# Performance work log

Hardware: AMD Instinct MI355X
Metric: run time of the kernel (lower is better)

## Reference

```python
import jax, jax.numpy as jnp
import numpy as np

B, T, E, H, V = 64, 128, 256, 1024, 8000

def setup_inputs() -> dict:
    key = jax.random.key(0)
    ks = jax.random.split(key, 18)
    s = 0.1
    f = lambda k, shp: (jax.random.normal(k, shp) * s).astype(jnp.float32)
    return {
        "x": jax.random.randint(ks[0], (B, T), 0, V),
        "given_num": 64,
        "emb": f(ks[1], (V, E)),
        "Wi": f(ks[2], (E, H)), "Ui": f(ks[3], (H, H)), "bi": f(ks[4], (H,)),
        "Wf": f(ks[5], (E, H)), "Uf": f(ks[6], (H, H)), "bf": f(ks[7], (H,)),
        "Wog": f(ks[8], (E, H)), "Uog": f(ks[9], (H, H)), "bog": f(ks[10], (H,)),
        "Wc": f(ks[11], (E, H)), "Uc": f(ks[12], (H, H)), "bc": f(ks[13], (H,)),
        "Wo": f(ks[14], (H, V)), "bo": f(ks[15], (V,)),
    }

def reference(x, given_num, emb, Wi, Ui, bi, Wf, Uf, bf, Wog, Uog, bog, Wc, Uc, bc, Wo, bo):
    # NOTE: the torch source overwrites processed_x[i] AFTER it has been consumed,
    # so the recurrence is fully teacher-forced on x; sampling only fills gen_x
    # for steps >= given_num. We reproduce exactly that.
    px = jnp.transpose(emb[x], (1, 0, 2))               # [T,B,E] teacher embeddings
    Wcat = jnp.concatenate([Wi, Wf, Wog, Wc], axis=1)    # [E,4H] fused input-gate weights
    Ucat = jnp.concatenate([Ui, Uf, Uog, Uc], axis=1)    # [H,4H] fused hidden-gate weights
    bcat = jnp.concatenate([bi, bf, bog, bc])            # [4H]
    xw = jnp.einsum('tbe,eh->tbh', px, Wcat) + bcat      # [T,B,4H] one big GEMM upfront
    keys = jax.random.split(jax.random.key(1), T)        # per-step sampling keys

    def step(carry, inp):
        h, c = carry
        xw_t, i, xtok, k = inp
        z = xw_t + h @ Ucat                              # [B,4H] fused gate pre-activations
        i_g, f_g, o_g, c_hat = jnp.split(z, 4, axis=-1)
        c = jax.nn.sigmoid(f_g) * c + jax.nn.sigmoid(i_g) * jnp.tanh(c_hat)
        h = jax.nn.sigmoid(o_g) * jnp.tanh(c)
        logits = h @ Wo + bo                             # [B,V]
        samp = jax.random.categorical(k, logits)         # = multinomial over softmax
        tok = jnp.where(i < given_num, xtok, samp)
        return (h, c), tok

    h0 = jnp.zeros((B, H), jnp.float32)
    c0 = jnp.zeros((B, H), jnp.float32)
    _, toks = jax.lax.scan(step, (h0, c0), (xw, jnp.arange(T), x.T, keys))
    return toks.T                                        # [B,T] int tokens (gen_x)
```

## Files before the change

### kernel.cpp

```cpp
#include <hip/hip_runtime.h>
#include <hip/hip_cooperative_groups.h>
#include <cstdint>
#include <cstddef>

#define TT 128
#define BB 64
#define EE 256
#define HH 1024
#define VV 8000
#define LSTRIDE 132

__device__ __forceinline__ uint32_t rotl32(uint32_t v, int r){ return (v<<r)|(v>>(32-r)); }

__device__ __forceinline__ void tf2x32(uint32_t k0, uint32_t k1, uint32_t x0, uint32_t x1,
                                       uint32_t& y0, uint32_t& y1)
{
  const uint32_t k2 = k0 ^ k1 ^ 0x1BD11BDAu;
  x0 += k0; x1 += k1;
#define TFR(r) { x0 += x1; x1 = rotl32(x1,(r)); x1 ^= x0; }
  TFR(13) TFR(15) TFR(26) TFR(6)   x0 += k1; x1 += k2 + 1u;
  TFR(17) TFR(29) TFR(16) TFR(24)  x0 += k2; x1 += k0 + 2u;
  TFR(13) TFR(15) TFR(26) TFR(6)   x0 += k0; x1 += k1 + 3u;
  TFR(17) TFR(29) TFR(16) TFR(24)  x0 += k1; x1 += k2 + 4u;
  TFR(13) TFR(15) TFR(26) TFR(6)   x0 += k2; x1 += k0 + 5u;
#undef TFR
  y0 = x0; y1 = x1;
}

__device__ __forceinline__ float u01f(uint32_t bits){
  float f = __uint_as_float((bits >> 9) | 0x3f800000u) - 1.0f;
  return (f == 0.0f) ? 1.17549435e-38f : f;
}

__device__ __forceinline__ float xla_tanh(float x){
  float xc = fminf(fmaxf(x, -7.90531110763549805f), 7.90531110763549805f);
  float x2 = __fmul_rn(xc, xc);
  float num = -2.76076847742355e-16f;
  num = __fadd_rn(__fmul_rn(x2, num),  2.00018790482477e-13f);
  num = __fadd_rn(__fmul_rn(x2, num), -8.60467152213735e-11f);
  num = __fadd_rn(__fmul_rn(x2, num),  5.12229709037114e-08f);
  num = __fadd_rn(__fmul_rn(x2, num),  1.48572235717979e-05f);
  num = __fadd_rn(__fmul_rn(x2, num),  6.37261928875436e-04f);
  num = __fadd_rn(__fmul_rn(x2, num),  4.89352455891786e-03f);
  num = __fmul_rn(xc, num);
  float den = 1.19825839466702e-06f;
  den = __fadd_rn(__fmul_rn(x2, den), 1.18534705686654e-04f);
  den = __fadd_rn(__fmul_rn(x2, den), 2.26843463243900e-03f);
  den = __fadd_rn(__fmul_rn(x2, den), 4.89352518554385e-03f);
  float r = __fdiv_rn(num, den);
  return (fabsf(x) < 0.0004f) ? x : r;
}

__device__ __forceinline__ float xla_sigmoid(float x){
  float t = xla_tanh(__fmul_rn(0.5f, x));
  return __fadd_rn(0.5f, __fmul_rn(0.5f, t));
}

__device__ __forceinline__ unsigned long long pack32(float s, int v){
  uint32_t u = __float_as_uint(s);
  u = (u >> 31) ? ~u : (u | 0x80000000u);
  return ((unsigned long long)u << 32) | (unsigned)(8191 - v);
}

#define LGKM0 asm volatile("s_waitcnt lgkmcnt(0)" ::: "memory")

__global__ void initz(float* hfull, unsigned long long* best, int* flags){
  int i = blockIdx.x*256 + threadIdx.x;
  if (i < HH*BB)  hfull[i] = 0.f;
  if (i < TT*BB)  best[i] = 0ull;
  if (i < 256)    flags[i] = 0;
}

__global__ __launch_bounds__(256) void pxgen(
    const int* __restrict__ x, const float* __restrict__ emb, float* __restrict__ px)
{
  int flat = blockIdx.x*256 + threadIdx.x;
  int b = flat & 63;
  int e = (flat >> 6) & 255;
  int t = flat >> 14;
  if (t >= TT) return;
  int tok = x[b*TT + t];
  px[((size_t)t*EE + e)*BB + b] = emb[(size_t)tok*EE + e];
}

__global__ __launch_bounds__(256) void transpose4f(
    const float* __restrict__ g0, const float* __restrict__ g1,
    const float* __restrict__ g2, const float* __restrict__ g3,
    float* __restrict__ out, int R, int C)
{
  const float* in = (blockIdx.y==0)?g0:(blockIdx.y==1)?g1:(blockIdx.y==2)?g2:g3;
  int tilesC = C >> 6;
  int tr = blockIdx.x / tilesC, tc = blockIdx.x % tilesC;
  __shared__ float tile[64][65];
  int tid = threadIdx.x;
  #pragma unroll
  for (int s = 0; s < 16; ++s) {
    int li = s*256 + tid;
    int r = li >> 6, c = li & 63;
    tile[r][c] = in[(size_t)(tr*64 + r)*C + tc*64 + c];
  }
  __syncthreads();
  #pragma unroll
  for (int s = 0; s < 16; ++s) {
    int li = s*256 + tid;
    int c = li >> 6, r = li & 63;
    out[((size_t)blockIdx.y*C + tc*64 + c)*R + tr*64 + r] = tile[r][c];
  }
}

__global__ __launch_bounds__(512, 2) void lstm_rec(
    const float* __restrict__ Wt, const float* __restrict__ Ut,
    const float* __restrict__ bi, const float* __restrict__ bf,
    const float* __restrict__ bog, const float* __restrict__ bc,
    const float* __restrict__ px, float* __restrict__ hfull,
    int* __restrict__ flags)
{
  __shared__ float sA[64*LSTRIDE];
  __shared__ float sB[64*LSTRIDE];
  __shared__ float spx[64*LSTRIDE];
  __shared__ float xch[512];

  const int tid  = threadIdx.x;
  const int w    = tid >> 6;
  const int lane = tid & 63;
  const int p    = w >> 1;
  const int half = w & 1;
  const int ju   = __builtin_amdgcn_readfirstlane(blockIdx.x*4 + p);
  const int g0   = 2*half, g1 = 2*half + 1;
  const int sw4  = ((lane >> 3) & 7) << 2;

  const float* U0 = Ut + ((size_t)g0*HH + ju)*HH;
  const float* U1 = Ut + ((size_t)g1*HH + ju)*HH;
  const float* W0 = Wt + ((size_t)g0*HH + ju)*EE;
  const float* W1 = Wt + ((size_t)g1*HH + ju)*EE;
  const float biaA = half ? bog[ju] : bi[ju];
  const float biaB = half ? bc[ju]  : bf[ju];

  float c = 0.f;
  float B0 = 0.f, B1 = 0.f;
  float4 pre[4];

  auto load_chunk = [&](const float* hp, int hcn){
    #pragma unroll
    for (int s = 0; s < 4; ++s) {
      int f = s*512 + tid;
      int k = f >> 4, b0 = (f & 15)*4;
      pre[s] = *(const float4*)(hp + (size_t)(hcn*128 + k)*BB + b0);
    }
  };
  auto store_chunk = [&](float* buf){
    #pragma unroll
    for (int s = 0; s < 4; ++s) {
      int f = s*512 + tid;
      int k = f >> 4, b0 = (f & 15)*4;
      int kc = k ^ (((b0 >> 3) & 7) << 2);
      buf[(b0+0)*LSTRIDE + kc] = pre[s].x;
      buf[(b0+1)*LSTRIDE + kc] = pre[s].y;
      buf[(b0+2)*LSTRIDE + kc] = pre[s].z;
      buf[(b0+3)*LSTRIDE + kc] = pre[s].w;
    }
  };

  auto compute_xw = [&](int t2){
    float A0 = 0.f, A1 = 0.f;
    #pragma unroll 1
    for (int ch = 0; ch < 2; ++ch) {
      const float* pxc = px + ((size_t)t2*EE + ch*128)*BB;
      LGKM0;
      __builtin_amdgcn_s_barrier();
      #pragma unroll
      for (int s = 0; s < 4; ++s) {
        int f = s*512 + tid;
        int e = f >> 4, b0 = (f & 15)*4;
        float4 v = *(const float4*)(pxc + (size_t)e*BB + b0);
        int ec = e ^ (((b0 >> 3) & 7) << 2);
        spx[(b0+0)*LSTRIDE + ec] = v.x;
        spx[(b0+1)*LSTRIDE + ec] = v.y;
        spx[(b0+2)*LSTRIDE + ec] = v.z;
        spx[(b0+3)*LSTRIDE + ec] = v.w;
      }
      LGKM0;
      __builtin_amdgcn_s_barrier();
      #pragma unroll
      for (int e = 0; e < 128; e += 4) {
        float4 p4 = *(const float4*)&spx[lane*LSTRIDE + (e ^ sw4)];
        A0 = __fadd_rn(A0, __fmul_rn(p4.x, W0[ch*128 + e + 0]));
        A1 = __fadd_rn(A1, __fmul_rn(p4.x, W1[ch*128 + e + 0]));
        A0 = __fadd_rn(A0, __fmul_rn(p4.y, W0[ch*128 + e + 1]));
        A1 = __fadd_rn(A1, __fmul_rn(p4.y, W1[ch*128 + e + 1]));
        A0 = __fadd_rn(A0, __fmul_rn(p4.z, W0[ch*128 + e + 2]));
        A1 = __fadd_rn(A1, __fmul_rn(p4.z, W1[ch*128 + e + 2]));
        A0 = __fadd_rn(A0, __fmul_rn(p4.w, W0[ch*128 + e + 3]));
        A1 = __fadd_rn(A1, __fmul_rn(p4.w, W1[ch*128 + e + 3]));
      }
    }
    B0 = __fadd_rn(A0, biaA);
    B1 = __fadd_rn(A1, biaB);
  };

  compute_xw(0);

  #pragma unroll 1
  for (int t = 0; t < TT; ++t) {
    const float* hp = hfull + (size_t)t*(HH*BB);
    float*       rn = hfull + (size_t)(t+1)*(HH*BB);

    load_chunk(hp, 0);
    float R0 = 0.f, R1 = 0.f, T0 = 0.f, T1 = 0.f;
    #pragma unroll 1
    for (int hc = 0; hc < 8; ++hc) {
      float* cur = (hc & 1) ? sB : sA;
      store_chunk(cur);
      if (hc < 7) load_chunk(hp, hc + 1);
      LGKM0;
      __builtin_amdgcn_s_barrier();
      #pragma unroll
      for (int sub = 0; sub < 4; ++sub) {
        int kabs = hc*128 + sub*32;
        if (kabs == 288 || kabs == 576 || kabs == 864) {
          T0 = __fadd_rn(T0, R0); R0 = 0.f;
          T1 = __fadd_rn(T1, R1); R1 = 0.f;
        }
        #pragma unroll
        for (int q = sub*32; q < sub*32 + 32; q += 4) {
          float4 h4 = *(const float4*)&cur[lane*LSTRIDE + (q ^ sw4)];
          R0 = __fadd_rn(R0, __fmul_rn(h4.x, U0[hc*128 + q + 0]));
          R1 = __fadd_rn(R1, __fmul_rn(h4.x, U1[hc*128 + q + 0]));
          R0 = __fadd_rn(R0, __fmul_rn(h4.y, U0[hc*128 + q + 1]));
          R1 = __fadd_rn(R1, __fmul_rn(h4.y, U1[hc*128 + q + 1]));
          R0 = __fadd_rn(R0, __fmul_rn(h4.z, U0[hc*128 + q + 2]));
          R1 = __fadd_rn(R1, __fmul_rn(h4.z, U1[hc*128 + q + 2]));
          R0 = __fadd_rn(R0, __fmul_rn(h4.w, U0[hc*128 + q + 3]));
          R1 = __fadd_rn(R1, __fmul_rn(h4.w, U1[hc*128 + q + 3]));
        }
      }
    }
    T0 = __fadd_rn(T0, R0);
    T1 = __fadd_rn(T1, R1);
    float z0 = __fadd_rn(B0, T0);
    float z1 = __fadd_rn(B1, T1);

    float igv = 0.f, fgv = 0.f, hv = 0.f;
    if (half) {
      float th  = xla_tanh(z1);
      float ogs = xla_sigmoid(z0);
      xch[p*64 + lane]       = th;
      xch[256 + p*64 + lane] = ogs;
    } else {
      igv = xla_sigmoid(z0);
      fgv = xla_sigmoid(z1);
    }
    LGKM0;
    __builtin_amdgcn_s_barrier();
    if (!half) {
      float th  = xch[p*64 + lane];
      float ogs = xch[256 + p*64 + lane];
      c = __fadd_rn(__fmul_rn(fgv, c), __fmul_rn(igv, th));
      hv = __fmul_rn(ogs, xla_tanh(c));
      __hip_atomic_store(&rn[(size_t)ju*BB + lane], hv,
                         __ATOMIC_RELAXED, __HIP_MEMORY_SCOPE_AGENT);
    }
    __syncthreads();
    if (tid == 0)
      __hip_atomic_store(&flags[blockIdx.x], t+1, __ATOMIC_RELEASE, __HIP_MEMORY_SCOPE_AGENT);

    if (t < TT-1) {
      compute_xw(t+1);
      if (w == 0) {
        for (;;) {
          int m0 = __hip_atomic_load(&flags[lane],       __ATOMIC_RELAXED, __HIP_MEMORY_SCOPE_AGENT);
          int m1 = __hip_atomic_load(&flags[64 + lane],  __ATOMIC_RELAXED, __HIP_MEMORY_SCOPE_AGENT);
          int m2 = __hip_atomic_load(&flags[128 + lane], __ATOMIC_RELAXED, __HIP_MEMORY_SCOPE_AGENT);
          int m3 = __hip_atomic_load(&flags[192 + lane], __ATOMIC_RELAXED, __HIP_MEMORY_SCOPE_AGENT);
          int mm = m0 < m1 ? m0 : m1;
          int nn = m2 < m3 ? m2 : m3;
          mm = mm < nn ? mm : nn;
          if (__all(mm >= t+1)) break;
          __builtin_amdgcn_s_sleep(1);
        }
        __atomic_signal_fence(__ATOMIC_ACQUIRE);
      }
      __syncthreads();
    }
  }
}

__global__ __launch_bounds__(256, 2) void logits_samp(
    const float* __restrict__ hfull, const float* __restrict__ Wo,
    const float* __restrict__ bo, const int* __restrict__ gnp,
    unsigned long long* __restrict__ best)
{
  const int t = 64 + blockIdx.y;
  if (t < gnp[0]) return;
  const int vt   = blockIdx.x;
  const int z    = blockIdx.z;
  const int tid  = threadIdx.x;
  const int w    = tid >> 6;
  const int lane = tid & 63;

  int v[4], vc[4]; bool val[4];
  #pragma unroll
  for (int vj = 0; vj < 4; ++vj) {
    v[vj]  = vt*1024 + vj*256 + tid;
    val[vj] = (v[vj] < VV);
    vc[vj] = val[vj] ? v[vj] : (VV-1);
  }

  __shared__ float hds[128*16];
  __shared__ unsigned long long red[4][16];

  float tot[64], reg[64];
  #pragma unroll
  for (int i = 0; i < 64; ++i) { tot[i] = 0.f; reg[i] = 0.f; }

  const float* hf = hfull + (size_t)(t+1)*(HH*BB);

  #pragma unroll 1
  for (int kc8 = 0; kc8 < 8; ++kc8) {
    __syncthreads();
    #pragma unroll
    for (int s = 0; s < 8; ++s) {
      int idx = s*256 + tid;
      int kl = idx >> 4, bb = idx & 15;
      hds[idx] = hf[(size_t)(kc8*128 + kl)*BB + z*16 + bb];
    }
    __syncthreads();
    #pragma unroll 1
    for (int sub = 0; sub < 4; ++sub) {
      int kabs = kc8*128 + sub*32;
      if (kabs == 288 || kabs == 576 || kabs == 864) {
        #pragma unroll
        for (int i = 0; i < 64; ++i) { tot[i] = __fadd_rn(tot[i], reg[i]); reg[i] = 0.f; }
      }
      #pragma unroll 2
      for (int k = sub*32; k < sub*32 + 32; ++k) {
        const float* wr = Wo + (size_t)(kc8*128 + k)*VV;
        float wv0 = wr[vc[0]], wv1 = wr[vc[1]], wv2 = wr[vc[2]], wv3 = wr[vc[3]];
        #pragma unroll
        for (int bb = 0; bb < 16; ++bb) {
          float hb = hds[k*16 + bb];
          reg[0*16+bb] = __fadd_rn(reg[0*16+bb], __fmul_rn(hb, wv0));
          reg[1*16+bb] = __fadd_rn(reg[1*16+bb], __fmul_rn(hb, wv1));
          reg[2*16+bb] = __fadd_rn(reg[2*16+bb], __fmul_rn(hb, wv2));
          reg[3*16+bb] = __fadd_rn(reg[3*16+bb], __fmul_rn(hb, wv3));
        }
      }
    }
  }
  #pragma unroll
  for (int i = 0; i < 64; ++i) tot[i] = __fadd_rn(tot[i], reg[i]);

  uint32_t kt0, kt1;
  tf2x32(0u, 1u, 0u, (uint32_t)t, kt0, kt1);
  float bov[4];
  #pragma unroll
  for (int vj = 0; vj < 4; ++vj) bov[vj] = val[vj] ? bo[v[vj]] : 0.f;

  #pragma unroll 1
  for (int bb = 0; bb < 16; ++bb) {
    int bglob = z*16 + bb;
    unsigned long long pm = 0ull;
    #pragma unroll
    for (int vj = 0; vj < 4; ++vj) {
      if (val[vj]) {
        uint32_t y0, y1;
        tf2x32(kt0, kt1, 0u, (uint32_t)(bglob*VV + v[vj]), y0, y1);
        float u  = u01f(y0 ^ y1);
        float l1 = logf(u);
        float l2 = logf(-l1);
        float g  = -l2;
        float L  = __fadd_rn(tot[vj*16 + bb], bov[vj]);
        float sc = __fadd_rn(g, L);
        unsigned long long pk = pack32(sc, v[vj]);
        if (pk > pm) pm = pk;
      }
    }
    #pragma unroll
    for (int m = 32; m > 0; m >>= 1) {
      unsigned long long q = __shfl_xor(pm, m);
      if (q > pm) pm = q;
    }
    if (lane == 0) red[w][bb] = pm;
    __syncthreads();
    if (tid == 0) {
      unsigned long long m0 = red[0][bb];
      if (red[1][bb] > m0) m0 = red[1][bb];
      if (red[2][bb] > m0) m0 = red[2][bb];
      if (red[3][bb] > m0) m0 = red[3][bb];
      atomicMax(&best[(size_t)t*BB + z*16 + bb], m0);
    }
    __syncthreads();
  }
}

__global__ void finalize(const int* __restrict__ x, const int* __restrict__ gnp,
                         const unsigned long long* __restrict__ best, int* __restrict__ out)
{
  int i = blockIdx.x*256 + threadIdx.x;
  if (i >= BB*TT) return;
  int t = i & 127;
  int b = i >> 7;
  if (t < gnp[0] || t < 64) out[i] = x[i];
  else out[i] = 8191 - (int)(best[(size_t)t*BB + b] & 0x1FFFull);
}

extern "C" void kernel_launch(void* const* d_in, const int* in_sizes, int n_in,
                              void* d_out, int out_size, void* d_ws, size_t ws_size,
                              hipStream_t stream)
{
  const int*   x    = (const int*)  d_in[0];
  const int*   gn   = (const int*)  d_in[1];
  const float* emb  = (const float*)d_in[2];
  const float* Wi   = (const float*)d_in[3];
  const float* Ui   = (const float*)d_in[4];
  const float* bi   = (const float*)d_in[5];
  const float* Wf   = (const float*)d_in[6];
  const float* Uf   = (const float*)d_in[7];
  const float* bf   = (const float*)d_in[8];
  const float* Wog  = (const float*)d_in[9];
  const float* Uog  = (const float*)d_in[10];
  const float* bog  = (const float*)d_in[11];
  const float* Wc   = (const float*)d_in[12];
  const float* Uc   = (const float*)d_in[13];
  const float* bc   = (const float*)d_in[14];
  const float* Wo   = (const float*)d_in[15];
  const float* bo   = (const float*)d_in[16];

  float* Ut    = (float*)d_ws;
  float* Wt    = Ut + (size_t)4*1024*1024;
  float* hfull = Wt + (size_t)1024*1024;
  float* px    = hfull + (size_t)(TT+1)*HH*BB;
  unsigned long long* best =
      (unsigned long long*)(px + (size_t)TT*EE*BB);
  int* flags  = (int*)(best + (size_t)TT*BB);

  initz<<<512, 256, 0, stream>>>(hfull, best, flags);
  transpose4f<<<dim3(256,4), 256, 0, stream>>>(Ui, Uf, Uog, Uc, Ut, 1024, 1024);
  transpose4f<<<dim3(64,4),  256, 0, stream>>>(Wi, Wf, Wog, Wc, Wt, 256, 1024);
  pxgen<<<8192, 256, 0, stream>>>(x, emb, px);

  const float* Wtp = Wt; const float* Utp = Ut;
  const float* bip = bi; const float* bfp = bf; const float* bogp = bog; const float* bcp = bc;
  const float* pxp = px; float* hfullp = hfull; int* flagsp = flags;
  void* kargs[] = { (void*)&Wtp, (void*)&Utp,
                    (void*)&bip, (void*)&bfp, (void*)&bogp, (void*)&bcp,
                    (void*)&pxp, (void*)&hfullp, (void*)&flagsp };
  hipLaunchCooperativeKernel((void*)lstm_rec, dim3(256), dim3(512), kargs, 0, stream);

  logits_samp<<<dim3(8,64,4), 256, 0, stream>>>(hfull, Wo, bo, gn, best);
  finalize<<<32, 256, 0, stream>>>(x, gn, best, (int*)d_out);
}
```

Measured before the change: 7.400 ms.

## Store h and px in lane-friendly blocked layout, drop LDS staging in recurrence

The hidden state and embedding inputs are rewritten into a blocked [t][b/16][k/4][b%16][k%4] layout, so each lane can read its float4 directly from global memory (L2). This replaces the shared-memory transpose staging, double buffering and barriers in the recurrent matvec and the input projection. A separate hist buffer in the original [k][b] layout is written for steps >= 64 so the logits kernel keeps its access pattern. The cost is more global/L2 traffic per step, with 16 redundant reads across waves, plus extra history stores.

After: 8.952 ms. 21.0% more time.

```diff
diff --git a/kernel.cpp b/kernel.cpp
--- a/kernel.cpp
+++ b/kernel.cpp
@@ -8,7 +8,6 @@
 #define EE 256
 #define HH 1024
 #define VV 8000
-#define LSTRIDE 132
 
 __device__ __forceinline__ uint32_t rotl32(uint32_t v, int r){ return (v<<r)|(v>>(32-r)); }
 
@@ -64,23 +63,24 @@
 
 #define LGKM0 asm volatile("s_waitcnt lgkmcnt(0)" ::: "memory")
 
-__global__ void initz(float* hfull, unsigned long long* best, int* flags){
+__global__ void initz(float* hT, unsigned long long* best, int* flags){
   int i = blockIdx.x*256 + threadIdx.x;
-  if (i < HH*BB)  hfull[i] = 0.f;
+  if (i < HH*BB)  hT[i] = 0.f;
   if (i < TT*BB)  best[i] = 0ull;
   if (i < 256)    flags[i] = 0;
 }
 
 __global__ __launch_bounds__(256) void pxgen(
-    const int* __restrict__ x, const float* __restrict__ emb, float* __restrict__ px)
+    const int* __restrict__ x, const float* __restrict__ emb, float* __restrict__ pxT)
 {
   int flat = blockIdx.x*256 + threadIdx.x;
-  int b = flat & 63;
-  int e = (flat >> 6) & 255;
+  int e = flat & 255;
+  int b = (flat >> 8) & 63;
   int t = flat >> 14;
   if (t >= TT) return;
   int tok = x[b*TT + t];
-  px[((size_t)t*EE + e)*BB + b] = emb[(size_t)tok*EE + e];
+  size_t fi = ((((size_t)t*4 + (b>>4))*64 + (e>>2))*16 + (size_t)(b&15))*4 + (e&3);
+  pxT[fi] = emb[(size_t)tok*EE + e];
 }
 
 __global__ __launch_bounds__(256) void transpose4f(
@@ -112,12 +112,9 @@
     const float* __restrict__ Wt, const float* __restrict__ Ut,
     const float* __restrict__ bi, const float* __restrict__ bf,
     const float* __restrict__ bog, const float* __restrict__ bc,
-    const float* __restrict__ px, float* __restrict__ hfull,
-    int* __restrict__ flags)
-{
-  __shared__ float sA[64*LSTRIDE];
-  __shared__ float sB[64*LSTRIDE];
-  __shared__ float spx[64*LSTRIDE];
+    const float* __restrict__ pxT, float* __restrict__ hT,
+    float* __restrict__ hist, int* __restrict__ flags)
+{
   __shared__ float xch[512];
 
   const int tid  = threadIdx.x;
@@ -127,7 +124,7 @@
   const int half = w & 1;
   const int ju   = __builtin_amdgcn_readfirstlane(blockIdx.x*4 + p);
   const int g0   = 2*half, g1 = 2*half + 1;
-  const int sw4  = ((lane >> 3) & 7) << 2;
+  const int lgrp = lane >> 4, l16 = lane & 15;
 
   const float* U0 = Ut + ((size_t)g0*HH + ju)*HH;
   const float* U1 = Ut + ((size_t)g1*HH + ju)*HH;
@@ -138,60 +135,25 @@
 
   float c = 0.f;
   float B0 = 0.f, B1 = 0.f;
-  float4 pre[4];
-
-  auto load_chunk = [&](const float* hp, int hcn){
-    #pragma unroll
-    for (int s = 0; s < 4; ++s) {
-      int f = s*512 + tid;
-      int k = f >> 4, b0 = (f & 15)*4;
-      pre[s] = *(const float4*)(hp + (size_t)(hcn*128 + k)*BB + b0);
-    }
-  };
-  auto store_chunk = [&](float* buf){
-    #pragma unroll
-    for (int s = 0; s < 4; ++s) {
-      int f = s*512 + tid;
-      int k = f >> 4, b0 = (f & 15)*4;
-      int kc = k ^ (((b0 >> 3) & 7) << 2);
-      buf[(b0+0)*LSTRIDE + kc] = pre[s].x;
-      buf[(b0+1)*LSTRIDE + kc] = pre[s].y;
-      buf[(b0+2)*LSTRIDE + kc] = pre[s].z;
-      buf[(b0+3)*LSTRIDE + kc] = pre[s].w;
-    }
-  };
 
   auto compute_xw = [&](int t2){
     float A0 = 0.f, A1 = 0.f;
+    const float4* pb = (const float4*)pxT + (((size_t)t2*4 + lgrp)*64)*16 + l16;
     #pragma unroll 1
-    for (int ch = 0; ch < 2; ++ch) {
-      const float* pxc = px + ((size_t)t2*EE + ch*128)*BB;
-      LGKM0;
-      __builtin_amdgcn_s_barrier();
+    for (int ec = 0; ec < 8; ++ec) {
       #pragma unroll
-      for (int s = 0; s < 4; ++s) {
-        int f = s*512 + tid;
-        int e = f >> 4, b0 = (f & 15)*4;
-        float4 v = *(const float4*)(pxc + (size_t)e*BB + b0);
-        int ec = e ^ (((b0 >> 3) & 7) << 2);
-        spx[(b0+0)*LSTRIDE + ec] = v.x;
-        spx[(b0+1)*LSTRIDE + ec] = v.y;
-        spx[(b0+2)*LSTRIDE + ec] = v.z;
-        spx[(b0+3)*LSTRIDE + ec] = v.w;
-      }
-      LGKM0;
-      __builtin_amdgcn_s_barrier();
-      #pragma unroll
-      for (int e = 0; e < 128; e += 4) {
-        float4 p4 = *(const float4*)&spx[lane*LSTRIDE + (e ^ sw4)];
-        A0 = __fadd_rn(A0, __fmul_rn(p4.x, W0[ch*128 + e + 0]));
-        A1 = __fadd_rn(A1, __fmul_rn(p4.x, W1[ch*128 + e + 0]));
-        A0 = __fadd_rn(A0, __fmul_rn(p4.y, W0[ch*128 + e + 1]));
-        A1 = __fadd_rn(A1, __fmul_rn(p4.y, W1[ch*128 + e + 1]));
-        A0 = __fadd_rn(A0, __fmul_rn(p4.z, W0[ch*128 + e + 2]));
-        A1 = __fadd_rn(A1, __fmul_rn(p4.z, W1[ch*128 + e + 2]));
-        A0 = __fadd_rn(A0, __fmul_rn(p4.w, W0[ch*128 + e + 3]));
-        A1 = __fadd_rn(A1, __fmul_rn(p4.w, W1[ch*128 + e + 3]));
+      for (int j = 0; j < 8; ++j) {
+        int eq = ec*8 + j;
+        float4 v = pb[(size_t)eq*16];
+        int e = eq*4;
+        A0 = __fadd_rn(A0, __fmul_rn(v.x, W0[e+0]));
+        A1 = __fadd_rn(A1, __fmul_rn(v.x, W1[e+0]));
+        A0 = __fadd_rn(A0, __fmul_rn(v.y, W0[e+1]));
+        A1 = __fadd_rn(A1, __fmul_rn(v.y, W1[e+1]));
+        A0 = __fadd_rn(A0, __fmul_rn(v.z, W0[e+2]));
+        A1 = __fadd_rn(A1, __fmul_rn(v.z, W1[e+2]));
+        A0 = __fadd_rn(A0, __fmul_rn(v.w, W0[e+3]));
+        A1 = __fadd_rn(A1, __fmul_rn(v.w, W1[e+3]));
       }
     }
     B0 = __fadd_rn(A0, biaA);
@@ -202,18 +164,10 @@
 
   #pragma unroll 1
   for (int t = 0; t < TT; ++t) {
-    const float* hp = hfull + (size_t)t*(HH*BB);
-    float*       rn = hfull + (size_t)(t+1)*(HH*BB);
-
-    load_chunk(hp, 0);
+    const float4* hb = (const float4*)hT + (((size_t)t*4 + lgrp)*256)*16 + l16;
     float R0 = 0.f, R1 = 0.f, T0 = 0.f, T1 = 0.f;
     #pragma unroll 1
     for (int hc = 0; hc < 8; ++hc) {
-      float* cur = (hc & 1) ? sB : sA;
-      store_chunk(cur);
-      if (hc < 7) load_chunk(hp, hc + 1);
-      LGKM0;
-      __builtin_amdgcn_s_barrier();
       #pragma unroll
       for (int sub = 0; sub < 4; ++sub) {
         int kabs = hc*128 + sub*32;
@@ -222,16 +176,18 @@
           T1 = __fadd_rn(T1, R1); R1 = 0.f;
         }
         #pragma unroll
-        for (int q = sub*32; q < sub*32 + 32; q += 4) {
-          float4 h4 = *(const float4*)&cur[lane*LSTRIDE + (q ^ sw4)];
-          R0 = __fadd_rn(R0, __fmul_rn(h4.x, U0[hc*128 + q + 0]));
-          R1 = __fadd_rn(R1, __fmul_rn(h4.x, U1[hc*128 + q + 0]));
-          R0 = __fadd_rn(R0, __fmul_rn(h4.y, U0[hc*128 + q + 1]));
-          R1 = __fadd_rn(R1, __fmul_rn(h4.y, U1[hc*128 + q + 1]));
-          R0 = __fadd_rn(R0, __fmul_rn(h4.z, U0[hc*128 + q + 2]));
-          R1 = __fadd_rn(R1, __fmul_rn(h4.z, U1[hc*128 + q + 2]));
-          R0 = __fadd_rn(R0, __fmul_rn(h4.w, U0[hc*128 + q + 3]));
-          R1 = __fadd_rn(R1, __fmul_rn(h4.w, U1[hc*128 + q + 3]));
+        for (int j = 0; j < 8; ++j) {
+          int kq = hc*32 + sub*8 + j;
+          float4 h4 = hb[(size_t)kq*16];
+          int k = kq*4;
+          R0 = __fadd_rn(R0, __fmul_rn(h4.x, U0[k+0]));
+          R1 = __fadd_rn(R1, __fmul_rn(h4.x, U1[k+0]));
+          R0 = __fadd_rn(R0, __fmul_rn(h4.y, U0[k+1]));
+          R1 = __fadd_rn(R1, __fmul_rn(h4.y, U1[k+1]));
+          R0 = __fadd_rn(R0, __fmul_rn(h4.z, U0[k+2]));
+          R1 = __fadd_rn(R1, __fmul_rn(h4.z, U1[k+2]));
+          R0 = __fadd_rn(R0, __fmul_rn(h4.w, U0[k+3]));
+          R1 = __fadd_rn(R1, __fmul_rn(h4.w, U1[k+3]));
         }
       }
     }
@@ -257,12 +213,14 @@
       float ogs = xch[256 + p*64 + lane];
       c = __fadd_rn(__fmul_rn(fgv, c), __fmul_rn(igv, th));
       hv = __fmul_rn(ogs, xla_tanh(c));
-      __hip_atomic_store(&rn[(size_t)ju*BB + lane], hv,
-                         __ATOMIC_RELAXED, __HIP_MEMORY_SCOPE_AGENT);
+      size_t fi = ((((size_t)(t+1)*4 + lgrp)*256 + (ju>>2))*16 + (size_t)l16)*4 + (ju&3);
+      __hip_atomic_store(&hT[fi], hv, __ATOMIC_RELAXED, __HIP_MEMORY_SCOPE_AGENT);
     }
     __syncthreads();
     if (tid == 0)
       __hip_atomic_store(&flags[blockIdx.x], t+1, __ATOMIC_RELEASE, __HIP_MEMORY_SCOPE_AGENT);
+    if (!half && t >= 64)
+      hist[(size_t)(t-64)*(HH*BB) + (size_t)ju*BB + lane] = hv;
 
     if (t < TT-1) {
       compute_xw(t+1);
@@ -286,7 +244,7 @@
 }
 
 __global__ __launch_bounds__(256, 2) void logits_samp(
-    const float* __restrict__ hfull, const float* __restrict__ Wo,
+    const float* __restrict__ hist, const float* __restrict__ Wo,
     const float* __restrict__ bo, const int* __restrict__ gnp,
     unsigned long long* __restrict__ best)
 {
@@ -313,7 +271,7 @@
   #pragma unroll
   for (int i = 0; i < 64; ++i) { tot[i] = 0.f; reg[i] = 0.f; }
 
-  const float* hf = hfull + (size_t)(t+1)*(HH*BB);
+  const float* hf = hist + (size_t)(t-64)*(HH*BB);
 
   #pragma unroll 1
   for (int kc8 = 0; kc8 < 8; ++kc8) {
@@ -428,25 +386,26 @@
 
   float* Ut    = (float*)d_ws;
   float* Wt    = Ut + (size_t)4*1024*1024;
-  float* hfull = Wt + (size_t)1024*1024;
-  float* px    = hfull + (size_t)(TT+1)*HH*BB;
+  float* hT    = Wt + (size_t)1024*1024;
+  float* hist  = hT + (size_t)(TT+1)*HH*BB;
+  float* pxT   = hist + (size_t)64*HH*BB;
   unsigned long long* best =
-      (unsigned long long*)(px + (size_t)TT*EE*BB);
+      (unsigned long long*)(pxT + (size_t)TT*EE*BB);
   int* flags  = (int*)(best + (size_t)TT*BB);
 
-  initz<<<512, 256, 0, stream>>>(hfull, best, flags);
+  initz<<<512, 256, 0, stream>>>(hT, best, flags);
   transpose4f<<<dim3(256,4), 256, 0, stream>>>(Ui, Uf, Uog, Uc, Ut, 1024, 1024);
   transpose4f<<<dim3(64,4),  256, 0, stream>>>(Wi, Wf, Wog, Wc, Wt, 256, 1024);
-  pxgen<<<8192, 256, 0, stream>>>(x, emb, px);
+  pxgen<<<8192, 256, 0, stream>>>(x, emb, pxT);
 
   const float* Wtp = Wt; const float* Utp = Ut;
   const float* bip = bi; const float* bfp = bf; const float* bogp = bog; const float* bcp = bc;
-  const float* pxp = px; float* hfullp = hfull; int* flagsp = flags;
+  const float* pxp = pxT; float* hTp = hT; float* histp = hist; int* flagsp = flags;
   void* kargs[] = { (void*)&Wtp, (void*)&Utp,
                     (void*)&bip, (void*)&bfp, (void*)&bogp, (void*)&bcp,
-                    (void*)&pxp, (void*)&hfullp, (void*)&flagsp };
+                    (void*)&pxp, (void*)&hTp, (void*)&histp, (void*)&flagsp };
   hipLaunchCooperativeKernel((void*)lstm_rec, dim3(256), dim3(512), kargs, 0, stream);
 
-  logits_samp<<<dim3(8,64,4), 256, 0, stream>>>(hfull, Wo, bo, gn, best);
+  logits_samp<<<dim3(8,64,4), 256, 0, stream>>>(hist, Wo, bo, gn, best);
   finalize<<<32, 256, 0, stream>>>(x, gn, best, (int*)d_out);
 }
```

## Split recurrent matvec by K-range across waves instead of by gate pair

Applied to the files above, without the earlier changes.

Each wave now computes all four gate partial sums over half of the hidden dimension, instead of two gates over the full dimension. Partial sums are exchanged through shared memory to rebuild the same rounding order as before. This balances the U reads and changes the register and LDS use per wave. It also drops the launch-bounds occupancy hint of two blocks. The cost is an extra barrier and more LDS traffic per step.

Result: faster. 6.239 ms (median of 2 runs) (-15.7%).

```diff
diff --git a/kernel.cpp b/kernel.cpp
--- a/kernel.cpp
+++ b/kernel.cpp
@@ -108,7 +108,7 @@
   }
 }
 
-__global__ __launch_bounds__(512, 2) void lstm_rec(
+__global__ __launch_bounds__(512) void lstm_rec(
     const float* __restrict__ Wt, const float* __restrict__ Ut,
     const float* __restrict__ bi, const float* __restrict__ bf,
     const float* __restrict__ bog, const float* __restrict__ bc,
@@ -118,23 +118,25 @@
   __shared__ float sA[64*LSTRIDE];
   __shared__ float sB[64*LSTRIDE];
   __shared__ float spx[64*LSTRIDE];
-  __shared__ float xch[512];
+  __shared__ float xch[2304];
 
   const int tid  = threadIdx.x;
   const int w    = tid >> 6;
   const int lane = tid & 63;
-  const int p    = w >> 1;
-  const int half = w & 1;
+  const int p    = w & 3;
+  const int kh   = w >> 2;
   const int ju   = __builtin_amdgcn_readfirstlane(blockIdx.x*4 + p);
-  const int g0   = 2*half, g1 = 2*half + 1;
   const int sw4  = ((lane >> 3) & 7) << 2;
 
-  const float* U0 = Ut + ((size_t)g0*HH + ju)*HH;
-  const float* U1 = Ut + ((size_t)g1*HH + ju)*HH;
+  const float* Ug0 = Ut + ((size_t)0*HH + ju)*HH;
+  const float* Ug1 = Ut + ((size_t)1*HH + ju)*HH;
+  const float* Ug2 = Ut + ((size_t)2*HH + ju)*HH;
+  const float* Ug3 = Ut + ((size_t)3*HH + ju)*HH;
+  const int g0 = 2*kh, g1 = 2*kh + 1;
   const float* W0 = Wt + ((size_t)g0*HH + ju)*EE;
   const float* W1 = Wt + ((size_t)g1*HH + ju)*EE;
-  const float biaA = half ? bog[ju] : bi[ju];
-  const float biaB = half ? bc[ju]  : bf[ju];
+  const float biaA = kh ? bog[ju] : bi[ju];
+  const float biaB = kh ? bc[ju]  : bf[ju];
 
   float c = 0.f;
   float B0 = 0.f, B1 = 0.f;
@@ -206,7 +208,8 @@
     float*       rn = hfull + (size_t)(t+1)*(HH*BB);
 
     load_chunk(hp, 0);
-    float R0 = 0.f, R1 = 0.f, T0 = 0.f, T1 = 0.f;
+    float R0=0.f, R1=0.f, R2=0.f, R3=0.f;
+    float PA0=0.f, PA1=0.f, PA2=0.f, PA3=0.f;
     #pragma unroll 1
     for (int hc = 0; hc < 8; ++hc) {
       float* cur = (hc & 1) ? sB : sA;
@@ -214,47 +217,85 @@
       if (hc < 7) load_chunk(hp, hc + 1);
       LGKM0;
       __builtin_amdgcn_s_barrier();
+      int sLo = kh ? ((hc == 4) ? 2 : (hc > 4 ? 0 : 4)) : 0;
+      int sHi = kh ? ((hc >= 4) ? 4 : 0)               : ((hc < 4) ? 4 : (hc == 4 ? 2 : 0));
       #pragma unroll
       for (int sub = 0; sub < 4; ++sub) {
+        if (sub < sLo || sub >= sHi) continue;
         int kabs = hc*128 + sub*32;
-        if (kabs == 288 || kabs == 576 || kabs == 864) {
-          T0 = __fadd_rn(T0, R0); R0 = 0.f;
-          T1 = __fadd_rn(T1, R1); R1 = 0.f;
+        if (kabs == 288 || kabs == 864) {
+          PA0 = R0; R0 = 0.f;
+          PA1 = R1; R1 = 0.f;
+          PA2 = R2; R2 = 0.f;
+          PA3 = R3; R3 = 0.f;
         }
         #pragma unroll
         for (int q = sub*32; q < sub*32 + 32; q += 4) {
           float4 h4 = *(const float4*)&cur[lane*LSTRIDE + (q ^ sw4)];
-          R0 = __fadd_rn(R0, __fmul_rn(h4.x, U0[hc*128 + q + 0]));
-          R1 = __fadd_rn(R1, __fmul_rn(h4.x, U1[hc*128 + q + 0]));
-          R0 = __fadd_rn(R0, __fmul_rn(h4.y, U0[hc*128 + q + 1]));
-          R1 = __fadd_rn(R1, __fmul_rn(h4.y, U1[hc*128 + q + 1]));
-          R0 = __fadd_rn(R0, __fmul_rn(h4.z, U0[hc*128 + q + 2]));
-          R1 = __fadd_rn(R1, __fmul_rn(h4.z, U1[hc*128 + q + 2]));
-          R0 = __fadd_rn(R0, __fmul_rn(h4.w, U0[hc*128 + q + 3]));
-          R1 = __fadd_rn(R1, __fmul_rn(h4.w, U1[hc*128 + q + 3]));
+          int k = hc*128 + q;
+          R0 = __fadd_rn(R0, __fmul_rn(h4.x, Ug0[k+0]));
+          R1 = __fadd_rn(R1, __fmul_rn(h4.x, Ug1[k+0]));
+          R2 = __fadd_rn(R2, __fmul_rn(h4.x, Ug2[k+0]));
+          R3 = __fadd_rn(R3, __fmul_rn(h4.x, Ug3[k+0]));
+          R0 = __fadd_rn(R0, __fmul_rn(h4.y, Ug0[k+1]));
+          R1 = __fadd_rn(R1, __fmul_rn(h4.y, Ug1[k+1]));
+          R2 = __fadd_rn(R2, __fmul_rn(h4.y, Ug2[k+1]));
+          R3 = __fadd_rn(R3, __fmul_rn(h4.y, Ug3[k+1]));
+          R0 = __fadd_rn(R0, __fmul_rn(h4.z, Ug0[k+2]));
+          R1 = __fadd_rn(R1, __fmul_rn(h4.z, Ug1[k+2]));
+          R2 = __fadd_rn(R2, __fmul_rn(h4.z, Ug2[k+2]));
+          R3 = __fadd_rn(R3, __fmul_rn(h4.z, Ug3[k+2]));
+          R0 = __fadd_rn(R0, __fmul_rn(h4.w, Ug0[k+3]));
+          R1 = __fadd_rn(R1, __fmul_rn(h4.w, Ug1[k+3]));
+          R2 = __fadd_rn(R2, __fmul_rn(h4.w, Ug2[k+3]));
+          R3 = __fadd_rn(R3, __fmul_rn(h4.w, Ug3[k+3]));
         }
       }
     }
-    T0 = __fadd_rn(T0, R0);
-    T1 = __fadd_rn(T1, R1);
-    float z0 = __fadd_rn(B0, T0);
-    float z1 = __fadd_rn(B1, T1);
+    float keepA = 0.f, keepB = 0.f, keepC = 0.f, keepD = 0.f;
+    if (kh == 0) {
+      keepA = __fadd_rn(PA0, R0);
+      keepB = __fadd_rn(PA1, R1);
+      xch[1024 + p*64 + lane] = __fadd_rn(PA2, R2);
+      xch[1280 + p*64 + lane] = __fadd_rn(PA3, R3);
+    } else {
+      keepA = PA2; keepB = R2;
+      keepC = PA3; keepD = R3;
+      xch[   0 + p*64 + lane] = PA0;
+      xch[ 256 + p*64 + lane] = R0;
+      xch[ 512 + p*64 + lane] = PA1;
+      xch[ 768 + p*64 + lane] = R1;
+    }
+    LGKM0;
+    __builtin_amdgcn_s_barrier();
+    float z0, z1;
+    if (kh == 0) {
+      float T0 = __fadd_rn(__fadd_rn(keepA, xch[   0 + p*64 + lane]), xch[ 256 + p*64 + lane]);
+      float T1 = __fadd_rn(__fadd_rn(keepB, xch[ 512 + p*64 + lane]), xch[ 768 + p*64 + lane]);
+      z0 = __fadd_rn(B0, T0);
+      z1 = __fadd_rn(B1, T1);
+    } else {
+      float T2 = __fadd_rn(__fadd_rn(xch[1024 + p*64 + lane], keepA), keepB);
+      float T3 = __fadd_rn(__fadd_rn(xch[1280 + p*64 + lane], keepC), keepD);
+      z0 = __fadd_rn(B0, T2);
+      z1 = __fadd_rn(B1, T3);
+    }
 
     float igv = 0.f, fgv = 0.f, hv = 0.f;
-    if (half) {
+    if (kh) {
       float th  = xla_tanh(z1);
       float ogs = xla_sigmoid(z0);
-      xch[p*64 + lane]       = th;
-      xch[256 + p*64 + lane] = ogs;
+      xch[1536 + p*64 + lane] = th;
+      xch[1792 + p*64 + lane] = ogs;
     } else {
       igv = xla_sigmoid(z0);
       fgv = xla_sigmoid(z1);
     }
     LGKM0;
     __builtin_amdgcn_s_barrier();
-    if (!half) {
-      float th  = xch[p*64 + lane];
-      float ogs = xch[256 + p*64 + lane];
+    if (!kh) {
+      float th  = xch[1536 + p*64 + lane];
+      float ogs = xch[1792 + p*64 + lane];
       c = __fadd_rn(__fmul_rn(fgv, c), __fmul_rn(igv, th));
       hv = __fmul_rn(ogs, xla_tanh(c));
       __hip_atomic_store(&rn[(size_t)ju*BB + lane], hv,
```
